# Optimization experiments

Hardware: AMD Instinct MI355X
Metric: run time of the kernel (lower is better)

Reference implementation:

```python
import jax, jax.numpy as jnp
import numpy as np

EMB = 1280
MD = 200
N = 20000
E = 200000
LN_EPS = 1e-5


def _layer_norm(x, g, b):
    mu = jnp.mean(x, axis=-1, keepdims=True)
    var = jnp.mean((x - mu) ** 2, axis=-1, keepdims=True)
    return (x - mu) * jax.lax.rsqrt(var + LN_EPS) * g + b


def _gat_conv(x, edge_index, edge_attr, W, We, a_src, a_dst, a_edge, bias, heads, C):
    """PyG GATConv (bias-free lin, edge_dim, add_self_loops with fill='mean')."""
    n = x.shape[0]
    src, dst = edge_index[0], edge_index[1]
    # self-loop edge_attr = mean of incoming edge_attr per dst node (0 if none)
    cnt = jax.ops.segment_sum(jnp.ones((edge_attr.shape[0],), x.dtype), dst, n)
    s = jax.ops.segment_sum(edge_attr, dst, n)
    loop_attr = jnp.where(cnt[:, None] > 0, s / jnp.maximum(cnt, 1.0)[:, None], 0.0)
    loop = jnp.arange(n)
    src = jnp.concatenate([src, loop])
    dst = jnp.concatenate([dst, loop])
    ea = jnp.concatenate([edge_attr, loop_attr], axis=0)
    h = (x @ W).reshape(n, heads, C)                      # [N,H,C]
    al_s = jnp.einsum('nhc,hc->nh', h, a_src)
    al_d = jnp.einsum('nhc,hc->nh', h, a_dst)
    eh = (ea @ We).reshape(-1, heads, C)                  # [E+N,H,C]
    al_e = jnp.einsum('ehc,hc->eh', eh, a_edge)
    alpha = jax.nn.leaky_relu(al_s[src] + al_d[dst] + al_e, 0.2)
    amax = jax.ops.segment_max(alpha, dst, n)
    amax = jnp.where(jnp.isfinite(amax), amax, 0.0)
    ex = jnp.exp(alpha - amax[dst])
    denom = jax.ops.segment_sum(ex, dst, n)
    w = ex / (denom[dst] + 1e-16)                         # segment softmax over dst
    out = jax.ops.segment_sum(h[src] * w[:, :, None], dst, n)
    return out.reshape(n, heads * C) + bias


def _forward(x, edge_index, edge_attr,
             ca_qw, ca_qb, ca_kw, ca_kb, ca_vw, ca_vb, ca_ow, ca_ob,
             g0_w, g0_ew, g0_as, g0_ad, g0_ae, g0_b, ln0_g, ln0_b,
             g1_w, g1_ew, g1_as, g1_ad, g1_ae, g1_b, ln1_g, ln1_b,
             g2_w, g2_ew, g2_as, g2_ad, g2_ae, g2_b, ln2_g, ln2_b,
             cls_w1, cls_b1, cls_w2, cls_b2):
    xe = x[:, :EMB]
    md = x[0, EMB:]
    # CrossAttention: single md vector -> K,V are [1,hidden]
    Q = xe @ ca_qw + ca_qb                                # [N,hid]
    K = md @ ca_kw + ca_kb                                # [hid]
    V = md @ ca_vw + ca_vb                                # [hid]
    scores = (Q @ K) / jnp.sqrt(jnp.asarray(Q.shape[-1], Q.dtype))  # [N]
    wts = jax.nn.softmax(scores, axis=0)[:, None]         # softmax over nodes
    attended = wts * V[None, :]                           # [N,hid]
    h = attended @ ca_ow + ca_ob + xe                     # [N,EMB]

    h = _gat_conv(h, edge_index, edge_attr, g0_w, g0_ew, g0_as, g0_ad, g0_ae, g0_b, 4, 256)
    h = jax.nn.relu(_layer_norm(h, ln0_g, ln0_b))
    h = _gat_conv(h, edge_index, edge_attr, g1_w, g1_ew, g1_as, g1_ad, g1_ae, g1_b, 4, 256)
    h = jax.nn.relu(_layer_norm(h, ln1_g, ln1_b))
    h = _gat_conv(h, edge_index, edge_attr, g2_w, g2_ew, g2_as, g2_ad, g2_ae, g2_b, 1, 256)
    h = jax.nn.relu(_layer_norm(h, ln2_g, ln2_b))

    g = jnp.mean(h, axis=0, keepdims=True)                # [1,256]
    g = jax.nn.relu(g @ cls_w1 + cls_b1)
    return g @ cls_w2 + cls_b2                            # [1,2]


def setup_inputs() -> dict:
    key = jax.random.key(0)
    ks = jax.random.split(key, 64)
    i = [0]
    def nrm(shape, scale=0.05):
        i[0] += 1
        return jax.random.normal(ks[i[0]], shape, jnp.float32) * scale
    inp = {}
    inp['x'] = nrm((N, EMB + MD), 1.0)
    inp['edge_index'] = jax.random.randint(ks[60], (2, E), 0, N, jnp.int64 if jax.config.read('jax_enable_x64') else jnp.int32)
    inp['edge_attr'] = jax.random.uniform(ks[61], (E, 1), jnp.float32)
    inp.update(ca_qw=nrm((EMB, 256)), ca_qb=jnp.zeros((256,), jnp.float32),
               ca_kw=nrm((MD, 256)), ca_kb=jnp.zeros((256,), jnp.float32),
               ca_vw=nrm((MD, 256)), ca_vb=jnp.zeros((256,), jnp.float32),
               ca_ow=nrm((256, EMB)), ca_ob=jnp.zeros((EMB,), jnp.float32))
    inp.update(g0_w=nrm((EMB, 1024)), g0_ew=nrm((1, 1024)), g0_as=nrm((4, 256)),
               g0_ad=nrm((4, 256)), g0_ae=nrm((4, 256)), g0_b=jnp.zeros((1024,), jnp.float32),
               ln0_g=jnp.ones((1024,), jnp.float32), ln0_b=jnp.zeros((1024,), jnp.float32))
    inp.update(g1_w=nrm((1024, 1024)), g1_ew=nrm((1, 1024)), g1_as=nrm((4, 256)),
               g1_ad=nrm((4, 256)), g1_ae=nrm((4, 256)), g1_b=jnp.zeros((1024,), jnp.float32),
               ln1_g=jnp.ones((1024,), jnp.float32), ln1_b=jnp.zeros((1024,), jnp.float32))
    inp.update(g2_w=nrm((1024, 256)), g2_ew=nrm((1, 256)), g2_as=nrm((1, 256)),
               g2_ad=nrm((1, 256)), g2_ae=nrm((1, 256)), g2_b=jnp.zeros((256,), jnp.float32),
               ln2_g=jnp.ones((256,), jnp.float32), ln2_b=jnp.zeros((256,), jnp.float32))
    inp.update(cls_w1=nrm((256, 128)), cls_b1=jnp.zeros((128,), jnp.float32),
               cls_w2=nrm((128, 2)), cls_b2=jnp.zeros((2,), jnp.float32))
    return inp


def reference(x, edge_index, edge_attr,
              ca_qw, ca_qb, ca_kw, ca_kb, ca_vw, ca_vb, ca_ow, ca_ob,
              g0_w, g0_ew, g0_as, g0_ad, g0_ae, g0_b, ln0_g, ln0_b,
              g1_w, g1_ew, g1_as, g1_ad, g1_ae, g1_b, ln1_g, ln1_b,
              g2_w, g2_ew, g2_as, g2_ad, g2_ae, g2_b, ln2_g, ln2_b,
              cls_w1, cls_b1, cls_w2, cls_b2):
    return _forward(x, edge_index, edge_attr,
                    ca_qw, ca_qb, ca_kw, ca_kb, ca_vw, ca_vb, ca_ow, ca_ob,
                    g0_w, g0_ew, g0_as, g0_ad, g0_ae, g0_b, ln0_g, ln0_b,
                    g1_w, g1_ew, g1_as, g1_ad, g1_ae, g1_b, ln1_g, ln1_b,
                    g2_w, g2_ew, g2_as, g2_ad, g2_ae, g2_b, ln2_g, ln2_b,
                    cls_w1, cls_b1, cls_w2, cls_b2)
```

## Files before the change

kernel.cpp:

```cpp
#include <hip/hip_runtime.h>
#include <hip/hip_bf16.h>
#include <math.h>

#define N_NODES 20000
#define N_EDGES 200000
#define XROW    1480

typedef __attribute__((ext_vector_type(8))) _Float16 f16x8;
typedef __attribute__((ext_vector_type(8))) unsigned short u16x8;
typedef __attribute__((ext_vector_type(4))) float f32x4v;

__device__ __forceinline__ float wsum(float v){
#pragma unroll
  for (int o=32;o>0;o>>=1) v += __shfl_down(v,o);
  return v;
}
__device__ __forceinline__ float wmax(float v){
#pragma unroll
  for (int o=32;o>0;o>>=1) v = fmaxf(v,__shfl_down(v,o));
  return v;
}
__device__ __forceinline__ float wsum_all(float v){
#pragma unroll
  for (int o=32;o>0;o>>=1) v += __shfl_xor(v,o);
  return v;
}
__device__ __forceinline__ float wmax_all(float v){
#pragma unroll
  for (int o=32;o>0;o>>=1) v = fmaxf(v,__shfl_xor(v,o));
  return v;
}

__device__ __forceinline__ unsigned short f2hu(float f){
  _Float16 h = (_Float16)f;
  return __builtin_bit_cast(unsigned short, h);
}
__device__ __forceinline__ float hu2f(unsigned short u){
  return (float)__builtin_bit_cast(_Float16, u);
}

__device__ __forceinline__ void async_copy16(void* lds, const void* g){
  __builtin_amdgcn_global_load_lds((const __attribute__((address_space(1))) void*)g,
                                   (__attribute__((address_space(3))) void*)lds, 16, 0, 0);
}

__global__ void edge_count_kernel(const int* __restrict__ ei, const float* __restrict__ ea,
                                  int* __restrict__ cnt, float* __restrict__ easum, int E){
  int e = blockIdx.x*256 + threadIdx.x;
  if (e >= E) return;
  int dst = ei[E + e];
  atomicAdd(&cnt[dst], 1);
  atomicAdd(&easum[dst], ea[e]);
}

__launch_bounds__(1024)
__global__ void scan_kernel(const int* __restrict__ cnt, const float* __restrict__ easum,
                            int* __restrict__ off, float* __restrict__ loop_attr, int n){
  __shared__ int buf[1024];
  __shared__ int carry_s;
  if (threadIdx.x==0) carry_s = 0;
  __syncthreads();
  for (int base=0; base<n; base+=1024){
    int i = base + threadIdx.x;
    int v = (i<n)? cnt[i] : 0;
    if (i<n){
      loop_attr[i] = (v>0) ? easum[i]/(float)v : 0.f;
    }
    buf[threadIdx.x] = v;
    __syncthreads();
    for (int d2=1; d2<1024; d2<<=1){
      int tv = (threadIdx.x>=d2)? buf[threadIdx.x-d2] : 0;
      __syncthreads();
      buf[threadIdx.x] += tv;
      __syncthreads();
    }
    if (i<n) off[i] = carry_s + buf[threadIdx.x] - v;
    int tot = buf[1023];
    __syncthreads();
    if (threadIdx.x==0) carry_s += tot;
    __syncthreads();
  }
  if (threadIdx.x==0) off[n] = carry_s;
}

__global__ void edge_fill_kernel(const int* __restrict__ ei, const float* __restrict__ ea,
                                 const int* __restrict__ off, int* __restrict__ fill,
                                 int* __restrict__ csr_src, float* __restrict__ csr_ea, int E){
  int e = blockIdx.x*256 + threadIdx.x;
  if (e >= E) return;
  int dst = ei[E + e];
  int pos = off[dst] + atomicAdd(&fill[dst], 1);
  csr_src[pos] = ei[e];
  csr_ea[pos]  = ea[e];
}

__global__ void x_to_f16(const float* __restrict__ x, unsigned short* __restrict__ xh){
  const int CH4 = 1280/4;
  long total = (long)N_NODES*CH4;
  for (long i = (long)blockIdx.x*256 + threadIdx.x; i < total; i += (long)gridDim.x*256){
    int row = (int)(i / CH4), c4 = (int)(i % CH4);
    float4 v = *(const float4*)(x + (size_t)row*XROW + c4*4);
    ushort4 o;
    o.x = f2hu(v.x); o.y = f2hu(v.y); o.z = f2hu(v.z); o.w = f2hu(v.w);
    *(ushort4*)(xh + (size_t)row*1280 + c4*4) = o;
  }
}

__global__ void wt_f16_kernel(const float* __restrict__ W, int K, int N,
                              unsigned short* __restrict__ Wt){
  __shared__ float tile[32][33];
  int k0 = blockIdx.x*32, n0 = blockIdx.y*32;
  int tx = threadIdx.x & 31, ty = threadIdx.x >> 5;
  for (int r=ty; r<32; r+=8) tile[r][tx] = W[(size_t)(k0+r)*N + n0+tx];
  __syncthreads();
  for (int r=ty; r<32; r+=8){
    float w = tile[tx][r];
    Wt[(size_t)(n0+r)*K + k0+tx] = f2hu(w);
  }
}

__global__ void kv_kernel(const float* __restrict__ x,
                          const float* __restrict__ kw, const float* __restrict__ kb,
                          const float* __restrict__ vw, const float* __restrict__ vb,
                          float* __restrict__ Kv, float* __restrict__ Vv){
  int j = threadIdx.x;
  float ka = kb[j], va = vb[j];
  for (int k=0;k<200;k++){
    float m = x[1280+k];
    ka = fmaf(m, kw[k*256+j], ka);
    va = fmaf(m, vw[k*256+j], va);
  }
  Kv[j]=ka; Vv[j]=va;
}

__global__ void qkvo_kernel(const float* __restrict__ qw, const float* __restrict__ ow,
                            const float* __restrict__ Kv, const float* __restrict__ Vv,
                            float* __restrict__ qK, float* __restrict__ Vo){
  int idx = blockIdx.x*256 + threadIdx.x;
  if (idx < 1280){
    float a=0;
    for (int j=0;j<256;j++) a = fmaf(qw[idx*256+j], Kv[j], a);
    qK[idx]=a;
  } else if (idx < 2560){
    int j = idx-1280;
    float a=0;
    for (int i=0;i<256;i++) a = fmaf(Vv[i], ow[(size_t)i*1280+j], a);
    Vo[j]=a;
  }
}

__global__ void obw_kernel(const float* __restrict__ ob, const float* __restrict__ Vo,
                           const float* __restrict__ W, float* __restrict__ obW, float* __restrict__ VoW){
  int j = blockIdx.x*256 + threadIdx.x;
  float a=0,b=0;
  for (int i=0;i<1280;i++){
    float w = W[(size_t)i*1024+j];
    a = fmaf(ob[i], w, a);
    b = fmaf(Vo[i], w, b);
  }
  obW[j]=a; VoW[j]=b;
}

__launch_bounds__(256)
__global__ void scores_kernel(const float* __restrict__ x, const float* __restrict__ qK,
                              float* __restrict__ scores, int n){
  __shared__ float qs[1280];
  int t = threadIdx.x;
  for (int i=t;i<1280;i+=256) qs[i]=qK[i];
  __syncthreads();
  int wid = t>>6, lane = t&63;
  int node = blockIdx.x*4 + wid;
  if (node >= n) return;
  const float4* row = (const float4*)(x + (size_t)node*XROW);
  float acc = 0;
#pragma unroll
  for (int it=0; it<5; it++){
    float4 v = row[lane + 64*it];
    float4 q = *(const float4*)&qs[4*(lane+64*it)];
    acc += v.x*q.x + v.y*q.y + v.z*q.z + v.w*q.w;
  }
  acc = wsum(acc);
  if (lane==0) scores[node] = acc;
}

__launch_bounds__(1024)
__global__ void softmax_nodes(const float* __restrict__ scores, float* __restrict__ wts, int n){
  __shared__ float red[16];
  int t = threadIdx.x, lane=t&63, wid=t>>6;
  float m = -INFINITY;
  for (int i=t;i<n;i+=1024) m = fmaxf(m, scores[i]);
  m = wmax(m);
  if (lane==0) red[wid]=m;
  __syncthreads();
  if (t==0){ float r=red[0]; for (int k=1;k<16;k++) r=fmaxf(r,red[k]); red[0]=r; }
  __syncthreads();
  float M = red[0];
  __syncthreads();
  float z=0;
  for (int i=t;i<n;i+=1024) z += expf((scores[i]-M)*(1.f/16.f));
  z = wsum(z);
  if (lane==0) red[wid]=z;
  __syncthreads();
  if (t==0){ float r=0; for (int k=0;k<16;k++) r+=red[k]; red[0]=r; }
  __syncthreads();
  float invZ = 1.f/red[0];
  for (int i=t;i<n;i+=1024) wts[i] = expf((scores[i]-M)*(1.f/16.f))*invZ;
}

__launch_bounds__(256)
__global__ void gemm_f16(const unsigned short* __restrict__ A,
                         const unsigned short* __restrict__ B,
                         unsigned short* __restrict__ C, int M, int N, int K,
                         const float* __restrict__ addCol,
                         const float* __restrict__ vCol,
                         const float* __restrict__ wRow)
{
  __shared__ short lds[2*128*64];
  short* As = lds;
  short* Bs = lds + 128*64;

  const int t = threadIdx.x;
  const int w = t>>6, l = t&63;
  const int bn = blockIdx.x*128, bm = blockIdx.y*128;
  const int wr = (w>>1)*64, wc = (w&1)*64;

  f32x4v acc[4][4];
#pragma unroll
  for (int i=0;i<4;i++)
#pragma unroll
    for (int j=0;j<4;j++) acc[i][j] = (f32x4v){0.f,0.f,0.f,0.f};

  const unsigned short* Ap[4]; const unsigned short* Bp[4];
  int ldsOff[4];
#pragma unroll
  for (int q=0;q<4;q++){
    int p  = (w*4+q)*64 + l;
    int r  = p>>3, pc = p&7;
    int kc = (pc ^ (r&7))*8;
    int rowA = bm + r; if (rowA > M-1) rowA = M-1;
    Ap[q] = A + (size_t)rowA*K + kc;
    Bp[q] = B + (size_t)(bn+r)*K + kc;
    ldsOff[q] = (w*4+q)*64*8;
  }

  for (int k0=0; k0<K; k0+=64){
#pragma unroll
    for (int q=0;q<4;q++) async_copy16(As + ldsOff[q], Ap[q] + k0);
#pragma unroll
    for (int q=0;q<4;q++) async_copy16(Bs + ldsOff[q], Bp[q] + k0);
    __syncthreads();

    const int q4 = l>>4, m16 = l&15;
#pragma unroll
    for (int ks=0; ks<2; ks++){
      f16x8 af[4], bf[4];
      const int c = ks*4 + q4;
#pragma unroll
      for (int i=0;i<4;i++){
        int ra = wr + i*16 + m16;
        af[i] = *(const f16x8*)&As[ra*64 + ((c ^ (ra&7))*8)];
        int rb = wc + i*16 + m16;
        bf[i] = *(const f16x8*)&Bs[rb*64 + ((c ^ (rb&7))*8)];
      }
#pragma unroll
      for (int i=0;i<4;i++)
#pragma unroll
        for (int j=0;j<4;j++)
          acc[i][j] = __builtin_amdgcn_mfma_f32_16x16x32_f16(af[i], bf[j], acc[i][j], 0,0,0);
    }
    __syncthreads();
  }

  const int q4 = l>>4, m16 = l&15;
#pragma unroll
  for (int i=0;i<4;i++){
#pragma unroll
    for (int r=0;r<4;r++){
      int m = bm + wr + i*16 + q4*4 + r;
      if (m >= M) continue;
      float wrow = addCol ? wRow[m] : 0.f;
      unsigned short* crow = C + (size_t)m*N;
#pragma unroll
      for (int j=0;j<4;j++){
        int n = bn + wc + j*16 + m16;
        float v = acc[i][j][r];
        if (addCol) v += addCol[n] + wrow*vCol[n];
        crow[n] = f2hu(v);
      }
    }
  }
}

template<int H>
__launch_bounds__(256)
__global__ void alsd_kernel(const unsigned short* __restrict__ h,
                            const float* __restrict__ a_src, const float* __restrict__ a_dst,
                            float* __restrict__ als, float* __restrict__ ald, int n){
  int gw = (blockIdx.x*256 + threadIdx.x) >> 6;
  int lane = threadIdx.x & 63;
  if (gw >= n*H) return;
  int node = gw / H, hd = gw % H;
  const ushort4* row = (const ushort4*)(h + (size_t)node*(256*H) + hd*256);
  const float4* as  = (const float4*)(a_src + hd*256);
  const float4* ad  = (const float4*)(a_dst + hd*256);
  ushort4 ru = row[lane];
  float4 a = as[lane], b = ad[lane];
  float rx=hu2f(ru.x), ry=hu2f(ru.y), rz=hu2f(ru.z), rw=hu2f(ru.w);
  float s = rx*a.x + ry*a.y + rz*a.z + rw*a.w;
  float d = rx*b.x + ry*b.y + rz*b.z + rw*b.w;
  s = wsum(s); d = wsum(d);
  if (lane==0){ als[(size_t)node*H+hd]=s; ald[(size_t)node*H+hd]=d; }
}

template<int H>
__global__ void we_kernel(const float* __restrict__ We, const float* __restrict__ a_edge,
                          float* __restrict__ we){
  int wid = threadIdx.x>>6, lane = threadIdx.x&63;
  if (wid < H){
    const float4* w4 = (const float4*)(We + wid*256);
    const float4* a4 = (const float4*)(a_edge + wid*256);
    float4 a = w4[lane], b = a4[lane];
    float v = a.x*b.x + a.y*b.y + a.z*b.z + a.w*b.w;
    v = wsum(v);
    if (lane==0) we[wid]=v;
  }
}

template<int H>
__launch_bounds__(256)
__global__ void gat_agg_ln_wave(const unsigned short* __restrict__ hmat,
                           const float* __restrict__ als, const float* __restrict__ ald,
                           const int* __restrict__ off, const int* __restrict__ csr_src,
                           const float* __restrict__ csr_ea, const float* __restrict__ loop_attr,
                           const float* __restrict__ we,
                           const float* __restrict__ bias,
                           const float* __restrict__ ln_g, const float* __restrict__ ln_b,
                           float* __restrict__ outf, unsigned short* __restrict__ outb, int n)
{
  constexpr int OUT = 256*H;
  constexpr int CPL = OUT/64;
  const int wv = threadIdx.x>>6, lane = threadIdx.x&63;
  const int i = blockIdx.x*4 + wv;
  __shared__ float wbuf_s[4][64*H];
  __shared__ int   sbuf_s[4][64];
  if (i >= n) return;
  float* wbuf = wbuf_s[wv];
  int*   sbuf = sbuf_s[wv];

  const int begin = off[i];
  const int deg   = off[i+1]-begin;
  const int S     = deg + 1;

  float aldi[H], wei[H];
#pragma unroll
  for (int hh=0;hh<H;hh++){ aldi[hh]=ald[(size_t)i*H+hh]; wei[hh]=we[hh]; }
  const float lea = loop_attr[i];

  const int head = (lane*CPL) >> 8;
  const int c0   = lane*CPL;
  float acc[CPL];
#pragma unroll
  for (int c=0;c<CPL;c++) acc[c]=0.f;

  if (S <= 64){
    int src = i; float ev = lea;
    if (lane < deg){ src = csr_src[begin+lane]; ev = csr_ea[begin+lane]; }
    const bool act = lane < S;
    float a[H];
#pragma unroll
    for (int hh=0;hh<H;hh++){
      float v = als[(size_t)src*H+hh] + aldi[hh] + ev*wei[hh];
      a[hh] = v>0.f ? v : 0.2f*v;
    }
#pragma unroll
    for (int hh=0;hh<H;hh++){
      float M = wmax_all(act ? a[hh] : -INFINITY);
      float e = act ? __expf(a[hh]-M) : 0.f;
      float Z = wsum_all(e);
      wbuf[lane*H+hh] = e / (Z + 1e-16f);
    }
    sbuf[lane] = src;
    for (int j=0;j<S;j++){
      int sj = sbuf[j];
      float wj = wbuf[j*H+head];
      const unsigned short* row = hmat + (size_t)sj*OUT + c0;
      if constexpr (CPL==16){
        u16x8 r0 = *(const u16x8*)(row);
        u16x8 r1 = *(const u16x8*)(row+8);
#pragma unroll
        for (int c=0;c<8;c++){
          acc[c]   = fmaf(wj, hu2f(r0[c]), acc[c]);
          acc[8+c] = fmaf(wj, hu2f(r1[c]), acc[8+c]);
        }
      } else {
        ushort4 r = *(const ushort4*)(row);
        acc[0]=fmaf(wj,hu2f(r.x),acc[0]); acc[1]=fmaf(wj,hu2f(r.y),acc[1]);
        acc[2]=fmaf(wj,hu2f(r.z),acc[2]); acc[3]=fmaf(wj,hu2f(r.w),acc[3]);
      }
    }
  } else {
    float rm[H];
#pragma unroll
    for (int hh=0;hh<H;hh++) rm[hh] = -INFINITY;
    for (int s=lane; s<S; s+=64){
      int src = (s<deg)? csr_src[begin+s] : i;
      float ev = (s<deg)? csr_ea[begin+s] : lea;
#pragma unroll
      for (int hh=0;hh<H;hh++){
        float v = als[(size_t)src*H+hh] + aldi[hh] + ev*wei[hh];
        v = v>0.f? v : 0.2f*v;
        rm[hh] = fmaxf(rm[hh], v);
      }
    }
    float M[H], es[H];
#pragma unroll
    for (int hh=0;hh<H;hh++){ M[hh]=wmax_all(rm[hh]); es[hh]=0.f; }
    for (int s=lane; s<S; s+=64){
      int src = (s<deg)? csr_src[begin+s] : i;
      float ev = (s<deg)? csr_ea[begin+s] : lea;
#pragma unroll
      for (int hh=0;hh<H;hh++){
        float v = als[(size_t)src*H+hh] + aldi[hh] + ev*wei[hh];
        v = v>0.f? v : 0.2f*v;
        es[hh] += __expf(v - M[hh]);
      }
    }
    float invZ[H];
#pragma unroll
    for (int hh=0;hh<H;hh++) invZ[hh] = 1.f/(wsum_all(es[hh]) + 1e-16f);
    for (int cb=0; cb<S; cb+=64){
      int m = min(64, S-cb);
      int s = cb + lane;
      if (s < S){
        int src = (s<deg)? csr_src[begin+s] : i;
        float ev = (s<deg)? csr_ea[begin+s] : lea;
        sbuf[lane] = src;
#pragma unroll
        for (int hh=0;hh<H;hh++){
          float v = als[(size_t)src*H+hh] + aldi[hh] + ev*wei[hh];
          v = v>0.f? v : 0.2f*v;
          wbuf[lane*H+hh] = __expf(v - M[hh]) * invZ[hh];
        }
      }
      for (int j=0;j<m;j++){
        int sj = sbuf[j];
        float wj = wbuf[j*H+head];
        const unsigned short* row = hmat + (size_t)sj*OUT + c0;
        if constexpr (CPL==16){
          u16x8 r0 = *(const u16x8*)(row);
          u16x8 r1 = *(const u16x8*)(row+8);
#pragma unroll
          for (int c=0;c<8;c++){
            acc[c]   = fmaf(wj, hu2f(r0[c]), acc[c]);
            acc[8+c] = fmaf(wj, hu2f(r1[c]), acc[8+c]);
          }
        } else {
          ushort4 r = *(const ushort4*)(row);
          acc[0]=fmaf(wj,hu2f(r.x),acc[0]); acc[1]=fmaf(wj,hu2f(r.y),acc[1]);
          acc[2]=fmaf(wj,hu2f(r.z),acc[2]); acc[3]=fmaf(wj,hu2f(r.w),acc[3]);
        }
      }
    }
  }

  float vals[CPL];
  float ls=0.f;
#pragma unroll
  for (int c=0;c<CPL;c+=4){
    float4 b4 = *(const float4*)(bias + c0 + c);
    vals[c]=acc[c]+b4.x; vals[c+1]=acc[c+1]+b4.y; vals[c+2]=acc[c+2]+b4.z; vals[c+3]=acc[c+3]+b4.w;
    ls += vals[c]+vals[c+1]+vals[c+2]+vals[c+3];
  }
  float mu = wsum_all(ls) * (1.f/OUT);
  float lv=0.f;
#pragma unroll
  for (int c=0;c<CPL;c++){ float d=vals[c]-mu; lv += d*d; }
  float inv = rsqrtf(wsum_all(lv)*(1.f/OUT) + 1e-5f);

  if (outb){
#pragma unroll
    for (int c=0;c<CPL;c+=8){
      u16x8 o;
#pragma unroll
      for (int k=0;k<8;k++){
        float g = ln_g[c0+c+k], b = ln_b[c0+c+k];
        o[k] = f2hu(fmaxf((vals[c+k]-mu)*inv*g + b, 0.f));
      }
      *(u16x8*)(outb + (size_t)i*OUT + c0 + c) = o;
    }
    if constexpr (CPL==4){
    }
  }
  if (outb && CPL==4){
    ushort4 o;
    o.x = f2hu(fmaxf((vals[0]-mu)*inv*ln_g[c0+0] + ln_b[c0+0], 0.f));
    o.y = f2hu(fmaxf((vals[1]-mu)*inv*ln_g[c0+1] + ln_b[c0+1], 0.f));
    o.z = f2hu(fmaxf((vals[2]-mu)*inv*ln_g[c0+2] + ln_b[c0+2], 0.f));
    o.w = f2hu(fmaxf((vals[3]-mu)*inv*ln_g[c0+3] + ln_b[c0+3], 0.f));
    *(ushort4*)(outb + (size_t)i*OUT + c0) = o;
  }
  if (!outb){
#pragma unroll
    for (int c=0;c<CPL;c+=4){
      float4 g4 = *(const float4*)(ln_g + c0 + c);
      float4 b4 = *(const float4*)(ln_b + c0 + c);
      float4 o;
      o.x = fmaxf((vals[c+0]-mu)*inv*g4.x + b4.x, 0.f);
      o.y = fmaxf((vals[c+1]-mu)*inv*g4.y + b4.y, 0.f);
      o.z = fmaxf((vals[c+2]-mu)*inv*g4.z + b4.z, 0.f);
      o.w = fmaxf((vals[c+3]-mu)*inv*g4.w + b4.w, 0.f);
      *(float4*)(outf + (size_t)i*OUT + c0 + c) = o;
    }
  }
}

__global__ void colsum_kernel(const float* __restrict__ h2, float* __restrict__ gsum, int n){
  int c = threadIdx.x;
  float acc=0;
  for (int i=blockIdx.x;i<n;i+=gridDim.x) acc += h2[(size_t)i*256 + c];
  atomicAdd(&gsum[c], acc);
}

__launch_bounds__(128)
__global__ void cls_kernel(const float* __restrict__ gsum,
                           const float* __restrict__ w1, const float* __restrict__ b1,
                           const float* __restrict__ w2, const float* __restrict__ b2,
                           float* __restrict__ outp){
  __shared__ float g[256];
  __shared__ float hid[128];
  int t = threadIdx.x;
  g[t]     = gsum[t]    *(1.f/N_NODES);
  g[t+128] = gsum[t+128]*(1.f/N_NODES);
  __syncthreads();
  float a = b1[t];
  for (int c=0;c<256;c++) a = fmaf(g[c], w1[c*128+t], a);
  hid[t] = fmaxf(a, 0.f);
  __syncthreads();
  if (t<2){
    float o = b2[t];
    for (int j=0;j<128;j++) o = fmaf(hid[j], w2[j*2+t], o);
    outp[t] = o;
  }
}

extern "C" void kernel_launch(void* const* d_in, const int* in_sizes, int n_in,
                              void* d_out, int out_size, void* d_ws, size_t ws_size,
                              hipStream_t stream)
{
  const float* x      = (const float*)d_in[0];
  const int*   ei     = (const int*)  d_in[1];
  const float* ea     = (const float*)d_in[2];
  const float* ca_qw  = (const float*)d_in[3];
  const float* ca_kw  = (const float*)d_in[5];
  const float* ca_kb  = (const float*)d_in[6];
  const float* ca_vw  = (const float*)d_in[7];
  const float* ca_vb  = (const float*)d_in[8];
  const float* ca_ow  = (const float*)d_in[9];
  const float* ca_ob  = (const float*)d_in[10];
  const float* g0_w   = (const float*)d_in[11];
  const float* g0_ew  = (const float*)d_in[12];
  const float* g0_as  = (const float*)d_in[13];
  const float* g0_ad  = (const float*)d_in[14];
  const float* g0_ae  = (const float*)d_in[15];
  const float* g0_b   = (const float*)d_in[16];
  const float* ln0_g  = (const float*)d_in[17];
  const float* ln0_b  = (const float*)d_in[18];
  const float* g1_w   = (const float*)d_in[19];
  const float* g1_ew  = (const float*)d_in[20];
  const float* g1_as  = (const float*)d_in[21];
  const float* g1_ad  = (const float*)d_in[22];
  const float* g1_ae  = (const float*)d_in[23];
  const float* g1_b   = (const float*)d_in[24];
  const float* ln1_g  = (const float*)d_in[25];
  const float* ln1_b  = (const float*)d_in[26];
  const float* g2_w   = (const float*)d_in[27];
  const float* g2_ew  = (const float*)d_in[28];
  const float* g2_as  = (const float*)d_in[29];
  const float* g2_ad  = (const float*)d_in[30];
  const float* g2_ae  = (const float*)d_in[31];
  const float* g2_b   = (const float*)d_in[32];
  const float* ln2_g  = (const float*)d_in[33];
  const float* ln2_b  = (const float*)d_in[34];
  const float* cls_w1 = (const float*)d_in[35];
  const float* cls_b1 = (const float*)d_in[36];
  const float* cls_w2 = (const float*)d_in[37];
  const float* cls_b2 = (const float*)d_in[38];
  float* outp = (float*)d_out;

  const int N = N_NODES, E = N_EDGES;

  char* base = (char*)d_ws;
  size_t o = 0;
  auto alloc = [&](size_t bytes)->void*{
    void* p = base + o;
    o += (bytes + 255) & ~(size_t)255;
    return p;
  };
  unsigned short* hF   = (unsigned short*)alloc((size_t)N*1024*2);
  unsigned short* Af   = (unsigned short*)alloc((size_t)N*1280*2);
  float*          h2   = (float*)         alloc((size_t)N*256*4);
  unsigned short* Wt   = (unsigned short*)alloc((size_t)1280*1024*2);
  float* als       = (float*)alloc((size_t)N*4*4);
  float* ald       = (float*)alloc((size_t)N*4*4);
  float* scores    = (float*)alloc((size_t)N*4);
  float* wts       = (float*)alloc((size_t)N*4);
  int*   cnt       = (int*)  alloc((size_t)N*4);
  float* easum     = (float*)alloc((size_t)N*4);
  int*   off       = (int*)  alloc((size_t)(N+1)*4);
  int*   fill      = (int*)  alloc((size_t)N*4);
  int*   csr_src   = (int*)  alloc((size_t)E*4);
  float* csr_ea    = (float*)alloc((size_t)E*4);
  float* loop_attr = (float*)alloc((size_t)N*4);
  float* Kv        = (float*)alloc(256*4);
  float* Vv        = (float*)alloc(256*4);
  float* qK        = (float*)alloc(1280*4);
  float* Vo        = (float*)alloc(1280*4);
  float* obW       = (float*)alloc(1024*4);
  float* VoW       = (float*)alloc(1024*4);
  float* web       = (float*)alloc(16*4);
  float* gsum      = (float*)alloc(256*4);

  hipMemsetAsync(cnt,   0, (size_t)N*4, stream);
  hipMemsetAsync(easum, 0, (size_t)N*4, stream);
  hipMemsetAsync(fill,  0, (size_t)N*4, stream);
  hipMemsetAsync(gsum,  0, 256*4,       stream);

  int eblocks = (E + 255)/256;
  edge_count_kernel<<<eblocks,256,0,stream>>>(ei, ea, cnt, easum, E);
  scan_kernel<<<1,1024,0,stream>>>(cnt, easum, off, loop_attr, N);
  edge_fill_kernel<<<eblocks,256,0,stream>>>(ei, ea, off, fill, csr_src, csr_ea, E);

  x_to_f16<<<2048,256,0,stream>>>(x, Af);

  kv_kernel<<<1,256,0,stream>>>(x, ca_kw, ca_kb, ca_vw, ca_vb, Kv, Vv);
  qkvo_kernel<<<10,256,0,stream>>>(ca_qw, ca_ow, Kv, Vv, qK, Vo);
  obw_kernel<<<4,256,0,stream>>>(ca_ob, Vo, g0_w, obW, VoW);
  scores_kernel<<<(N+3)/4,256,0,stream>>>(x, qK, scores, N);
  softmax_nodes<<<1,1024,0,stream>>>(scores, wts, N);

  const int MB = (N + 127)/128;
  const int NB4 = (N + 3)/4;

  wt_f16_kernel<<<dim3(1280/32, 1024/32),256,0,stream>>>(g0_w, 1280, 1024, Wt);
  gemm_f16<<<dim3(1024/128, MB),256,0,stream>>>(Af, Wt, hF, N, 1024, 1280, obW, VoW, wts);
  alsd_kernel<4><<<N,256,0,stream>>>(hF, g0_as, g0_ad, als, ald, N);
  we_kernel<4><<<1,256,0,stream>>>(g0_ew, g0_ae, web);
  gat_agg_ln_wave<4><<<NB4,256,0,stream>>>(hF, als, ald, off, csr_src, csr_ea, loop_attr,
                                           web, g0_b, ln0_g, ln0_b, nullptr, Af, N);

  wt_f16_kernel<<<dim3(1024/32, 1024/32),256,0,stream>>>(g1_w, 1024, 1024, Wt);
  gemm_f16<<<dim3(1024/128, MB),256,0,stream>>>(Af, Wt, hF, N, 1024, 1024, nullptr, nullptr, nullptr);
  alsd_kernel<4><<<N,256,0,stream>>>(hF, g1_as, g1_ad, als, ald, N);
  we_kernel<4><<<1,256,0,stream>>>(g1_ew, g1_ae, web);
  gat_agg_ln_wave<4><<<NB4,256,0,stream>>>(hF, als, ald, off, csr_src, csr_ea, loop_attr,
                                           web, g1_b, ln1_g, ln1_b, nullptr, Af, N);

  wt_f16_kernel<<<dim3(1024/32, 256/32),256,0,stream>>>(g2_w, 1024, 256, Wt);
  gemm_f16<<<dim3(256/128, MB),256,0,stream>>>(Af, Wt, hF, N, 256, 1024, nullptr, nullptr, nullptr);
  alsd_kernel<1><<<(N+3)/4,256,0,stream>>>(hF, g2_as, g2_ad, als, ald, N);
  we_kernel<1><<<1,256,0,stream>>>(g2_ew, g2_ae, web);
  gat_agg_ln_wave<1><<<NB4,256,0,stream>>>(hF, als, ald, off, csr_src, csr_ea, loop_attr,
                                           web, g2_b, ln2_g, ln2_b, h2, nullptr, N);

  colsum_kernel<<<256,256,0,stream>>>(h2, gsum, N);
  cls_kernel<<<1,128,0,stream>>>(gsum, cls_w1, cls_b1, cls_w2, cls_b2, outp);

  (void)in_sizes; (void)n_in; (void)out_size; (void)ws_size;
}
```

Baseline: 953.8 us.

## Fuse attention-logit dot products into GEMM epilogue and swizzle block order

Removes the separate alsd kernel. The GEMM epilogue now computes per-head a_src/a_dst dot products from the fp32 accumulators, reduces them across 16 lanes and atomically adds the results into zeroed als/ald buffers. The GEMM grid is also remapped so groups of 8 row bands share the same column tiles, which improves L2 reuse. In exchange it adds a memset and atomics per layer, uses unrounded fp32 values for the logits, and makes the summation order non-deterministic.

```diff
diff --git a/kernel.cpp b/kernel.cpp
--- a/kernel.cpp
+++ b/kernel.cpp
@@ -213,15 +213,27 @@
                          unsigned short* __restrict__ C, int M, int N, int K,
                          const float* __restrict__ addCol,
                          const float* __restrict__ vCol,
-                         const float* __restrict__ wRow)
+                         const float* __restrict__ wRow,
+                         const float* __restrict__ a_src,
+                         const float* __restrict__ a_dst,
+                         float* __restrict__ als,
+                         float* __restrict__ ald,
+                         int H)
 {
   __shared__ short lds[2*128*64];
   short* As = lds;
   short* Bs = lds + 128*64;
 
+  const int ntc = N >> 7;
+  const int sh  = __popc(ntc - 1);
+  const int g   = blockIdx.y >> sh;
+  const int nt  = blockIdx.y & (ntc - 1);
+  const int band = blockIdx.x + (g << 3);
+  if (band * 128 >= M) return;
+
   const int t = threadIdx.x;
   const int w = t>>6, l = t&63;
-  const int bn = blockIdx.x*128, bm = blockIdx.y*128;
+  const int bm = band*128, bn = nt*128;
   const int wr = (w>>1)*64, wc = (w&1)*64;
 
   f32x4v acc[4][4];
@@ -272,6 +284,14 @@
   }
 
   const int q4 = l>>4, m16 = l&15;
+  const int hd = (bn + wc) >> 8;
+  float asv[4], adv[4];
+#pragma unroll
+  for (int j=0;j<4;j++){
+    int n = bn + wc + j*16 + m16;
+    asv[j] = a_src[n];
+    adv[j] = a_dst[n];
+  }
 #pragma unroll
   for (int i=0;i<4;i++){
 #pragma unroll
@@ -280,36 +300,25 @@
       if (m >= M) continue;
       float wrow = addCol ? wRow[m] : 0.f;
       unsigned short* crow = C + (size_t)m*N;
+      float vj[4];
 #pragma unroll
       for (int j=0;j<4;j++){
         int n = bn + wc + j*16 + m16;
         float v = acc[i][j][r];
         if (addCol) v += addCol[n] + wrow*vCol[n];
+        vj[j] = v;
         crow[n] = f2hu(v);
       }
-    }
-  }
-}
-
-template<int H>
-__launch_bounds__(256)
-__global__ void alsd_kernel(const unsigned short* __restrict__ h,
-                            const float* __restrict__ a_src, const float* __restrict__ a_dst,
-                            float* __restrict__ als, float* __restrict__ ald, int n){
-  int gw = (blockIdx.x*256 + threadIdx.x) >> 6;
-  int lane = threadIdx.x & 63;
-  if (gw >= n*H) return;
-  int node = gw / H, hd = gw % H;
-  const ushort4* row = (const ushort4*)(h + (size_t)node*(256*H) + hd*256);
-  const float4* as  = (const float4*)(a_src + hd*256);
-  const float4* ad  = (const float4*)(a_dst + hd*256);
-  ushort4 ru = row[lane];
-  float4 a = as[lane], b = ad[lane];
-  float rx=hu2f(ru.x), ry=hu2f(ru.y), rz=hu2f(ru.z), rw=hu2f(ru.w);
-  float s = rx*a.x + ry*a.y + rz*a.z + rw*a.w;
-  float d = rx*b.x + ry*b.y + rz*b.z + rw*b.w;
-  s = wsum(s); d = wsum(d);
-  if (lane==0){ als[(size_t)node*H+hd]=s; ald[(size_t)node*H+hd]=d; }
+      float s = vj[0]*asv[0] + vj[1]*asv[1] + vj[2]*asv[2] + vj[3]*asv[3];
+      float d = vj[0]*adv[0] + vj[1]*adv[1] + vj[2]*adv[2] + vj[3]*adv[3];
+#pragma unroll
+      for (int o=1;o<16;o<<=1){ s += __shfl_xor(s,o); d += __shfl_xor(d,o); }
+      if (m16 == 0){
+        atomicAdd(&als[(size_t)m*H + hd], s);
+        atomicAdd(&ald[(size_t)m*H + hd], d);
+      }
+    }
+  }
 }
 
 template<int H>
@@ -600,8 +609,8 @@
   unsigned short* Af   = (unsigned short*)alloc((size_t)N*1280*2);
   float*          h2   = (float*)         alloc((size_t)N*256*4);
   unsigned short* Wt   = (unsigned short*)alloc((size_t)1280*1024*2);
-  float* als       = (float*)alloc((size_t)N*4*4);
-  float* ald       = (float*)alloc((size_t)N*4*4);
+  float* als       = (float*)alloc((size_t)2*N*4*4);
+  float* ald       = als + (size_t)N*4;
   float* scores    = (float*)alloc((size_t)N*4);
   float* wts       = (float*)alloc((size_t)N*4);
   int*   cnt       = (int*)  alloc((size_t)N*4);
@@ -638,26 +647,30 @@
   scores_kernel<<<(N+3)/4,256,0,stream>>>(x, qK, scores, N);
   softmax_nodes<<<1,1024,0,stream>>>(scores, wts, N);
 
-  const int MB = (N + 127)/128;
+  const int mTiles  = (N + 127)/128;
+  const int mGroups = (mTiles + 7)/8;
   const int NB4 = (N + 3)/4;
 
   wt_f16_kernel<<<dim3(1280/32, 1024/32),256,0,stream>>>(g0_w, 1280, 1024, Wt);
-  gemm_f16<<<dim3(1024/128, MB),256,0,stream>>>(Af, Wt, hF, N, 1024, 1280, obW, VoW, wts);
-  alsd_kernel<4><<<N,256,0,stream>>>(hF, g0_as, g0_ad, als, ald, N);
+  hipMemsetAsync(als, 0, (size_t)2*N*4*4, stream);
+  gemm_f16<<<dim3(8, mGroups*8),256,0,stream>>>(Af, Wt, hF, N, 1024, 1280, obW, VoW, wts,
+                                                g0_as, g0_ad, als, ald, 4);
   we_kernel<4><<<1,256,0,stream>>>(g0_ew, g0_ae, web);
   gat_agg_ln_wave<4><<<NB4,256,0,stream>>>(hF, als, ald, off, csr_src, csr_ea, loop_attr,
                                            web, g0_b, ln0_g, ln0_b, nullptr, Af, N);
 
   wt_f16_kernel<<<dim3(1024/32, 1024/32),256,0,stream>>>(g1_w, 1024, 1024, Wt);
-  gemm_f16<<<dim3(1024/128, MB),256,0,stream>>>(Af, Wt, hF, N, 1024, 1024, nullptr, nullptr, nullptr);
-  alsd_kernel<4><<<N,256,0,stream>>>(hF, g1_as, g1_ad, als, ald, N);
+  hipMemsetAsync(als, 0, (size_t)2*N*4*4, stream);
+  gemm_f16<<<dim3(8, mGroups*8),256,0,stream>>>(Af, Wt, hF, N, 1024, 1024, nullptr, nullptr, nullptr,
+                                                g1_as, g1_ad, als, ald, 4);
   we_kernel<4><<<1,256,0,stream>>>(g1_ew, g1_ae, web);
   gat_agg_ln_wave<4><<<NB4,256,0,stream>>>(hF, als, ald, off, csr_src, csr_ea, loop_attr,
                                            web, g1_b, ln1_g, ln1_b, nullptr, Af, N);
 
   wt_f16_kernel<<<dim3(1024/32, 256/32),256,0,stream>>>(g2_w, 1024, 256, Wt);
-  gemm_f16<<<dim3(256/128, MB),256,0,stream>>>(Af, Wt, hF, N, 256, 1024, nullptr, nullptr, nullptr);
-  alsd_kernel<1><<<(N+3)/4,256,0,stream>>>(hF, g2_as, g2_ad, als, ald, N);
+  hipMemsetAsync(als, 0, (size_t)2*N*4*4, stream);
+  gemm_f16<<<dim3(8, mGroups*2),256,0,stream>>>(Af, Wt, hF, N, 256, 1024, nullptr, nullptr, nullptr,
+                                                g2_as, g2_ad, als, ald, 1);
   we_kernel<1><<<1,256,0,stream>>>(g2_ew, g2_ae, web);
   gat_agg_ln_wave<1><<<NB4,256,0,stream>>>(hF, als, ald, off, csr_src, csr_ea, loop_attr,
                                            web, g2_b, ln2_g, ln2_b, h2, nullptr, N);
```

Measured after the change: 981.5 us. +2.9%, slower.
